# Optimization experiments

Hardware: AMD Instinct MI355X
Metric: run time of the kernel (lower is better)

Reference implementation:

```python
import jax, jax.numpy as jnp
import numpy as np

N, D, K = 10240, 256, 30  # nodes, feature dim, top-k
EPS = 1e-12  # F.normalize eps


def setup_inputs() -> dict:
    key = jax.random.key(0)
    k1, _ = jax.random.split(key)
    features = jax.random.normal(k1, (N, D), dtype=jnp.float32)
    # Attentive layers: elementwise feature weights, initialized to ones (as in the repo)
    w1 = jnp.ones((D,), dtype=jnp.float32)
    w2 = jnp.ones((D,), dtype=jnp.float32)
    return {"features": features, "w1": w1, "w2": w2, "k": K}


def reference(features, w1, w2, k):
    # internal_forward: Attentive = x * w (x @ diag(w)); relu between layers (mlp_act='relu')
    h = jax.nn.relu(features * w1) * w2              # [N, D]
    # F.normalize(dim=1, p=2) with eps clamp
    norm = jnp.maximum(jnp.linalg.norm(h, axis=1, keepdims=True), EPS)
    emb = h / norm                                   # [N, D]
    # cal_similarity_graph: dense cosine similarity
    sim = emb @ emb.T                                # [N, N]
    # top_k(sim, k+1): keep top (k+1) entries per row, zero the rest
    _, idx = jax.lax.top_k(sim, k + 1)               # [N, k+1]
    rows = jnp.arange(sim.shape[0])[:, None]
    mask = jnp.zeros_like(sim).at[rows, idx].set(1.0)
    # apply_non_linearity with 'relu'
    return jax.nn.relu(sim * mask)
```

## Files before the change

### kernel.cpp

```cpp
#include <hip/hip_runtime.h>
#include <math.h>

#define N_NODES 10240
#define DIM 256
#define TPB 256
#define CAP 1536

typedef _Float16 half8 __attribute__((ext_vector_type(8)));
typedef float f32x4 __attribute__((ext_vector_type(4)));

__device__ __forceinline__ void async_load16(const void* g, void* l) {
  __builtin_amdgcn_global_load_lds(
      (const __attribute__((address_space(1))) unsigned int*)g,
      (__attribute__((address_space(3))) unsigned int*)l, 16, 0, 0);
}

__device__ __forceinline__ unsigned int fmap(float f) {
  unsigned int s = __float_as_uint(f);
  return (s & 0x80000000u) ? ~s : (s | 0x80000000u);
}
__device__ __forceinline__ float funmap(unsigned int m) {
  return __uint_as_float((m & 0x80000000u) ? (m ^ 0x80000000u) : ~m);
}

__global__ __launch_bounds__(256) void norm_split_kernel(
    const float* __restrict__ F, const float* __restrict__ w1,
    const float* __restrict__ w2, _Float16* __restrict__ P0,
    _Float16* __restrict__ P1) {
  int row = blockIdx.x, tid = threadIdx.x;
  __shared__ float red[TPB];
  size_t base = (size_t)row * DIM + tid;
  float h = fmaxf(F[base] * w1[tid], 0.0f) * w2[tid];
  red[tid] = h * h;
  __syncthreads();
  for (int o = TPB / 2; o > 0; o >>= 1) {
    if (tid < o) red[tid] += red[tid + o];
    __syncthreads();
  }
  float e = h / fmaxf(sqrtf(red[0]), 1e-12f);
  _Float16 p0 = (_Float16)e;
  _Float16 p1 = (_Float16)((e - (float)p0) * 2048.0f);
  P0[base] = p0;
  P1[base] = p1;
}

__global__ __launch_bounds__(256) void gemm_mfma_kernel(
    const _Float16* __restrict__ P0, const _Float16* __restrict__ P1,
    float* __restrict__ C) {
  __shared__ char smem[32768];
  char* AsB = smem;
  char* BsB = smem + 16384;

  int tid = threadIdx.x;
  int lane = tid & 63;
  int w = tid >> 6;
  int wr = (w >> 1) * 64;
  int wc = (w & 1) * 64;
  int quad = lane >> 4;
  int mr = lane & 15;
  int rowBase = blockIdx.y * 128;
  int colBase = blockIdx.x * 128;

  size_t rowOffA[4], rowOffB[4];
  int ldsOff[4];
#pragma unroll
  for (int i = 0; i < 4; ++i) {
    int u = tid + i * 256;
    int m = u >> 3;
    int g = (u & 7) ^ (m & 7);
    ldsOff[i] = u * 16;
    rowOffA[i] = (size_t)(rowBase + m) * DIM + g * 8;
    rowOffB[i] = (size_t)(colBase + m) * DIM + g * 8;
  }

  int fOffA[2][4], fOffB[2][4];
#pragma unroll
  for (int s = 0; s < 2; ++s)
#pragma unroll
    for (int t = 0; t < 4; ++t) {
      int g = s * 4 + quad;
      int mA = wr + t * 16 + mr;
      fOffA[s][t] = (mA * 8 + (g ^ (mA & 7))) * 16;
      int mB = wc + t * 16 + mr;
      fOffB[s][t] = (mB * 8 + (g ^ (mB & 7))) * 16;
    }

  f32x4 acc[4][4];
#pragma unroll
  for (int t = 0; t < 4; ++t)
#pragma unroll
    for (int u2 = 0; u2 < 4; ++u2) acc[t][u2] = (f32x4)0.0f;

  const _Float16* Aseg[3] = {P0, P1, P0};
  const _Float16* Bseg[3] = {P1, P0, P0};

  for (int pass = 0; pass < 3; ++pass) {
    if (pass == 2) {
      const float sc = 1.0f / 2048.0f;
#pragma unroll
      for (int t = 0; t < 4; ++t)
#pragma unroll
        for (int u2 = 0; u2 < 4; ++u2)
#pragma unroll
          for (int r = 0; r < 4; ++r) acc[t][u2][r] *= sc;
    }
    const _Float16* Ap = Aseg[pass];
    const _Float16* Bp = Bseg[pass];
    for (int c = 0; c < 4; ++c) {
      int kb = c * 64;
#pragma unroll
      for (int i = 0; i < 4; ++i)
        async_load16(Ap + rowOffA[i] + kb, AsB + ldsOff[i]);
#pragma unroll
      for (int i = 0; i < 4; ++i)
        async_load16(Bp + rowOffB[i] + kb, BsB + ldsOff[i]);
      __syncthreads();
#pragma unroll
      for (int s = 0; s < 2; ++s) {
        half8 af[4], bf[4];
#pragma unroll
        for (int t = 0; t < 4; ++t) {
          af[t] = *(const half8*)(AsB + fOffA[s][t]);
          bf[t] = *(const half8*)(BsB + fOffB[s][t]);
        }
#pragma unroll
        for (int t = 0; t < 4; ++t)
#pragma unroll
          for (int u2 = 0; u2 < 4; ++u2)
            acc[t][u2] = __builtin_amdgcn_mfma_f32_16x16x32_f16(
                af[t], bf[u2], acc[t][u2], 0, 0, 0);
      }
      __syncthreads();
    }
  }

#pragma unroll
  for (int t = 0; t < 4; ++t) {
    int gr = rowBase + wr + t * 16 + quad * 4;
#pragma unroll
    for (int u2 = 0; u2 < 4; ++u2) {
      int gc = colBase + wc + u2 * 16 + mr;
      float* cp = C + (size_t)gr * N_NODES + gc;
      cp[0] = acc[t][u2][0];
      cp[(size_t)N_NODES] = acc[t][u2][1];
      cp[(size_t)2 * N_NODES] = acc[t][u2][2];
      cp[(size_t)3 * N_NODES] = acc[t][u2][3];
    }
  }
}

__global__ __launch_bounds__(256) void topk_sparse_kernel(
    const float* __restrict__ SIM, float* __restrict__ OUT,
    const int* __restrict__ kptr) {
  constexpr int EPT = N_NODES / TPB;
  constexpr int NV4 = EPT / 4;
  __shared__ unsigned int lm[TPB];
  __shared__ unsigned int cu[CAP];
  __shared__ int ci[CAP];
  __shared__ unsigned int s_cnt, s_L31, s_Tu;
  __shared__ int s_Jcut;

  int tid = threadIdx.x;
  const float* Srow = SIM + (size_t)blockIdx.x * N_NODES;
  float* Orow = OUT + (size_t)blockIdx.x * N_NODES;
  unsigned int want = (unsigned int)(kptr[0] + 1);

  unsigned int u[EPT];
  unsigned int lmax = 0u;
#pragma unroll
  for (int i = 0; i < NV4; ++i) {
    float4 v = *(const float4*)&Srow[(i * TPB + tid) * 4];
    float fv[4] = {v.x, v.y, v.z, v.w};
#pragma unroll
    for (int c = 0; c < 4; ++c) {
      unsigned int m = fmap(fv[c]);
      u[i * 4 + c] = m;
      lmax = (m > lmax) ? m : lmax;
    }
  }
  lm[tid] = lmax;
  if (tid == 0) s_cnt = 0u;
  __syncthreads();

  {
    unsigned int r = 0;
    for (int j = 0; j < TPB; ++j) {
      unsigned int vj = lm[j];
      r += (vj > lmax) || (vj == lmax && j < tid);
    }
    if (r == want - 1) s_L31 = lmax;
  }
  __syncthreads();
  unsigned int L31 = s_L31;

#pragma unroll
  for (int i = 0; i < EPT; ++i) {
    if (u[i] >= L31) {
      unsigned int pos = atomicAdd(&s_cnt, 1u);
      if (pos < CAP) {
        cu[pos] = u[i];
        ci[pos] = ((i / 4) * TPB + tid) * 4 + (i % 4);
      }
    }
  }
  __syncthreads();
  unsigned int c_total = s_cnt;

  if (c_total <= CAP) {
    for (unsigned int i = tid; i < c_total; i += TPB) {
      unsigned int ui = cu[i];
      int ii = ci[i];
      unsigned int r = 0;
      for (unsigned int j = 0; j < c_total; ++j) {
        unsigned int uj = cu[j];
        r += (uj > ui) || (uj == ui && ci[j] < ii);
      }
      if (r == want - 1) { s_Tu = ui; s_Jcut = ii; }
    }
    __syncthreads();
  } else {
    unsigned int lo = 0u, hi = 0xFFFFFFFFu;
    while (lo < hi) {
      unsigned int mid = lo + ((hi - lo) >> 1);
      unsigned int cnt = 0;
#pragma unroll
      for (int i = 0; i < EPT; ++i) cnt += (u[i] > mid) ? 1u : 0u;
      lm[tid] = cnt;
      __syncthreads();
      for (int o = TPB / 2; o > 0; o >>= 1) {
        if (tid < o) lm[tid] += lm[tid + o];
        __syncthreads();
      }
      unsigned int gcnt = lm[0];
      __syncthreads();
      if (gcnt < want) hi = mid; else lo = mid + 1u;
    }
    unsigned int Tu = lo;
    unsigned int cnt = 0;
#pragma unroll
    for (int i = 0; i < EPT; ++i) cnt += (u[i] > Tu) ? 1u : 0u;
    lm[tid] = cnt;
    __syncthreads();
    for (int o = TPB / 2; o > 0; o >>= 1) {
      if (tid < o) lm[tid] += lm[tid + o];
      __syncthreads();
    }
    unsigned int need = want - lm[0];
    __syncthreads();
    int jlo = 0, jhi = N_NODES - 1;
    while (jlo < jhi) {
      int jmid = (jlo + jhi) >> 1;
      unsigned int cc = 0;
#pragma unroll
      for (int i = 0; i < EPT; ++i) {
        int jj = ((i / 4) * TPB + tid) * 4 + (i % 4);
        cc += (u[i] == Tu && jj <= jmid) ? 1u : 0u;
      }
      lm[tid] = cc;
      __syncthreads();
      for (int o = TPB / 2; o > 0; o >>= 1) {
        if (tid < o) lm[tid] += lm[tid + o];
        __syncthreads();
      }
      unsigned int tot = lm[0];
      __syncthreads();
      if (tot >= need) jhi = jmid; else jlo = jmid + 1;
    }
    if (tid == 0) { s_Tu = Tu; s_Jcut = jlo; }
    __syncthreads();
  }

  unsigned int Tu = s_Tu;
  int Jcut = s_Jcut;

#pragma unroll
  for (int i = 0; i < EPT; ++i) {
    unsigned int m = u[i];
    int j = ((i / 4) * TPB + tid) * 4 + (i % 4);
    bool keep = (m > Tu) || (m == Tu && j <= Jcut);
    if (keep) {
      float v = funmap(m);
      if (v > 0.0f) Orow[j] = v;
    }
  }
}

__global__ __launch_bounds__(256) void topk_kernel(
    float* __restrict__ C, const int* __restrict__ kptr) {
  constexpr int EPT = N_NODES / TPB;
  constexpr int NV4 = EPT / 4;
  __shared__ unsigned int lm[TPB];
  __shared__ unsigned int cu[CAP];
  __shared__ int ci[CAP];
  __shared__ unsigned int s_cnt, s_L31, s_Tu;
  __shared__ int s_Jcut;

  int tid = threadIdx.x;
  float* Crow = C + (size_t)blockIdx.x * N_NODES;
  unsigned int want = (unsigned int)(kptr[0] + 1);

  unsigned int u[EPT];
  unsigned int lmax = 0u;
#pragma unroll
  for (int i = 0; i < NV4; ++i) {
    float4 v = *(const float4*)&Crow[(i * TPB + tid) * 4];
    float fv[4] = {v.x, v.y, v.z, v.w};
#pragma unroll
    for (int c = 0; c < 4; ++c) {
      unsigned int m = fmap(fv[c]);
      u[i * 4 + c] = m;
      lmax = (m > lmax) ? m : lmax;
    }
  }
  lm[tid] = lmax;
  if (tid == 0) s_cnt = 0u;
  __syncthreads();

  {
    unsigned int r = 0;
    for (int j = 0; j < TPB; ++j) {
      unsigned int vj = lm[j];
      r += (vj > lmax) || (vj == lmax && j < tid);
    }
    if (r == want - 1) s_L31 = lmax;
  }
  __syncthreads();
  unsigned int L31 = s_L31;

#pragma unroll
  for (int i = 0; i < EPT; ++i) {
    if (u[i] >= L31) {
      unsigned int pos = atomicAdd(&s_cnt, 1u);
      if (pos < CAP) {
        cu[pos] = u[i];
        ci[pos] = ((i / 4) * TPB + tid) * 4 + (i % 4);
      }
    }
  }
  __syncthreads();
  unsigned int c_total = s_cnt;

  if (c_total <= CAP) {
    for (unsigned int i = tid; i < c_total; i += TPB) {
      unsigned int ui = cu[i];
      int ii = ci[i];
      unsigned int r = 0;
      for (unsigned int j = 0; j < c_total; ++j) {
        unsigned int uj = cu[j];
        r += (uj > ui) || (uj == ui && ci[j] < ii);
      }
      if (r == want - 1) { s_Tu = ui; s_Jcut = ii; }
    }
    __syncthreads();
  } else {
    unsigned int lo = 0u, hi = 0xFFFFFFFFu;
    while (lo < hi) {
      unsigned int mid = lo + ((hi - lo) >> 1);
      unsigned int cnt = 0;
#pragma unroll
      for (int i = 0; i < EPT; ++i) cnt += (u[i] > mid) ? 1u : 0u;
      lm[tid] = cnt;
      __syncthreads();
      for (int o = TPB / 2; o > 0; o >>= 1) {
        if (tid < o) lm[tid] += lm[tid + o];
        __syncthreads();
      }
      unsigned int gcnt = lm[0];
      __syncthreads();
      if (gcnt < want) hi = mid; else lo = mid + 1u;
    }
    unsigned int Tu = lo;
    unsigned int cnt = 0;
#pragma unroll
    for (int i = 0; i < EPT; ++i) cnt += (u[i] > Tu) ? 1u : 0u;
    lm[tid] = cnt;
    __syncthreads();
    for (int o = TPB / 2; o > 0; o >>= 1) {
      if (tid < o) lm[tid] += lm[tid + o];
      __syncthreads();
    }
    unsigned int need = want - lm[0];
    __syncthreads();
    int jlo = 0, jhi = N_NODES - 1;
    while (jlo < jhi) {
      int jmid = (jlo + jhi) >> 1;
      unsigned int cc = 0;
#pragma unroll
      for (int i = 0; i < EPT; ++i) {
        int jj = ((i / 4) * TPB + tid) * 4 + (i % 4);
        cc += (u[i] == Tu && jj <= jmid) ? 1u : 0u;
      }
      lm[tid] = cc;
      __syncthreads();
      for (int o = TPB / 2; o > 0; o >>= 1) {
        if (tid < o) lm[tid] += lm[tid + o];
        __syncthreads();
      }
      unsigned int tot = lm[0];
      __syncthreads();
      if (tot >= need) jhi = jmid; else jlo = jmid + 1;
    }
    if (tid == 0) { s_Tu = Tu; s_Jcut = jlo; }
    __syncthreads();
  }

  unsigned int Tu = s_Tu;
  int Jcut = s_Jcut;

#pragma unroll
  for (int i = 0; i < NV4; ++i) {
    float out[4];
#pragma unroll
    for (int c = 0; c < 4; ++c) {
      unsigned int m = u[i * 4 + c];
      int j = (i * TPB + tid) * 4 + c;
      bool keep = (m > Tu) || (m == Tu && j <= Jcut);
      float v = funmap(m);
      out[c] = (keep && v > 0.0f) ? v : 0.0f;
    }
    *(float4*)&Crow[(i * TPB + tid) * 4] =
        make_float4(out[0], out[1], out[2], out[3]);
  }
}

extern "C" void kernel_launch(void* const* d_in, const int* in_sizes, int n_in,
                              void* d_out, int out_size, void* d_ws, size_t ws_size,
                              hipStream_t stream) {
  const float* F  = (const float*)d_in[0];
  const float* w1 = (const float*)d_in[1];
  const float* w2 = (const float*)d_in[2];
  const int*   kp = (const int*)d_in[3];
  float* C = (float*)d_out;
  _Float16* P0 = (_Float16*)d_ws;
  _Float16* P1 = P0 + (size_t)N_NODES * DIM;

  size_t pbytes = (size_t)N_NODES * DIM * sizeof(_Float16);
  size_t simoff = 2 * pbytes;
  size_t need = simoff + (size_t)N_NODES * N_NODES * sizeof(float);

  dim3 grid(N_NODES / 128, N_NODES / 128);

  norm_split_kernel<<<N_NODES, DIM, 0, stream>>>(F, w1, w2, P0, P1);

  if (ws_size >= need) {
    float* SIM = (float*)((char*)d_ws + simoff);
    gemm_mfma_kernel<<<grid, 256, 0, stream>>>(P0, P1, SIM);
    topk_sparse_kernel<<<N_NODES, TPB, 0, stream>>>(SIM, C, kp);
  } else {
    gemm_mfma_kernel<<<grid, 256, 0, stream>>>(P0, P1, C);
    topk_kernel<<<N_NODES, TPB, 0, stream>>>(C, kp);
  }
}
```

Measured before the change: 655.2 us.

## Emit per-tile row maxima from GEMM and prune top-k to candidate tiles

The GEMM epilogue now reduces each 128x128 tile's accumulators to a per-row maximum and writes these into an extra workspace array of 80 tile maxima per row. The top-k kernel ranks those 80 maxima to find a threshold and only reads the column tiles whose maximum reaches it, rather than streaming the full 10240-wide similarity row. Candidates are then ranked exactly and scattered from shared memory. It adds a shared-memory reduction and sync to the GEMM tail and needs more workspace, and it falls back to a full-row bisection when the candidate count overflows.

```diff
diff --git a/kernel.cpp b/kernel.cpp
--- a/kernel.cpp
+++ b/kernel.cpp
@@ -5,6 +5,8 @@
 #define DIM 256
 #define TPB 256
 #define CAP 1536
+#define CAP2 2048
+#define NTILE 80
 
 typedef _Float16 half8 __attribute__((ext_vector_type(8)));
 typedef float f32x4 __attribute__((ext_vector_type(4)));
@@ -46,8 +48,8 @@
 
 __global__ __launch_bounds__(256) void gemm_mfma_kernel(
     const _Float16* __restrict__ P0, const _Float16* __restrict__ P1,
-    float* __restrict__ C) {
-  __shared__ char smem[32768];
+    float* __restrict__ C, float* __restrict__ TM) {
+  __shared__ __align__(16) char smem[32768];
   char* AsB = smem;
   char* BsB = smem + 16384;
 
@@ -147,78 +149,116 @@
       cp[(size_t)3 * N_NODES] = acc[t][u2][3];
     }
   }
-}
-
-__global__ __launch_bounds__(256) void topk_sparse_kernel(
-    const float* __restrict__ SIM, float* __restrict__ OUT,
-    const int* __restrict__ kptr) {
+
+  if (TM != nullptr) {
+    float* red = (float*)smem;
+    int half = w & 1;
+#pragma unroll
+    for (int t = 0; t < 4; ++t)
+#pragma unroll
+      for (int r = 0; r < 4; ++r) {
+        float m = fmaxf(fmaxf(acc[t][0][r], acc[t][1][r]),
+                        fmaxf(acc[t][2][r], acc[t][3][r]));
+        m = fmaxf(m, __shfl_xor(m, 1, 64));
+        m = fmaxf(m, __shfl_xor(m, 2, 64));
+        m = fmaxf(m, __shfl_xor(m, 4, 64));
+        m = fmaxf(m, __shfl_xor(m, 8, 64));
+        if (mr == 0) red[half * 128 + wr + t * 16 + quad * 4 + r] = m;
+      }
+    __syncthreads();
+    if (tid < 64) {
+      float a0 = fmaxf(red[2 * tid], red[128 + 2 * tid]);
+      float a1 = fmaxf(red[2 * tid + 1], red[128 + 2 * tid + 1]);
+      *(float2*)(TM + (size_t)blockIdx.x * N_NODES + rowBase + 2 * tid) =
+          make_float2(a0, a1);
+    }
+  }
+}
+
+__global__ __launch_bounds__(256) void topk_tile_kernel(
+    const float* __restrict__ SIM, const float* __restrict__ TM,
+    float* __restrict__ OUT, const int* __restrict__ kptr) {
   constexpr int EPT = N_NODES / TPB;
   constexpr int NV4 = EPT / 4;
+  __shared__ unsigned int sm[NTILE];
+  __shared__ unsigned char qlist[NTILE];
+  __shared__ unsigned int cu[CAP2];
+  __shared__ int ci[CAP2];
   __shared__ unsigned int lm[TPB];
-  __shared__ unsigned int cu[CAP];
-  __shared__ int ci[CAP];
-  __shared__ unsigned int s_cnt, s_L31, s_Tu;
+  __shared__ unsigned int s_cnt, s_q, s_Tp, s_Tu;
   __shared__ int s_Jcut;
 
   int tid = threadIdx.x;
-  const float* Srow = SIM + (size_t)blockIdx.x * N_NODES;
-  float* Orow = OUT + (size_t)blockIdx.x * N_NODES;
+  int row = blockIdx.x;
+  const float* Srow = SIM + (size_t)row * N_NODES;
+  float* Orow = OUT + (size_t)row * N_NODES;
   unsigned int want = (unsigned int)(kptr[0] + 1);
 
-  unsigned int u[EPT];
-  unsigned int lmax = 0u;
-#pragma unroll
-  for (int i = 0; i < NV4; ++i) {
-    float4 v = *(const float4*)&Srow[(i * TPB + tid) * 4];
-    float fv[4] = {v.x, v.y, v.z, v.w};
-#pragma unroll
-    for (int c = 0; c < 4; ++c) {
-      unsigned int m = fmap(fv[c]);
-      u[i * 4 + c] = m;
-      lmax = (m > lmax) ? m : lmax;
-    }
-  }
-  lm[tid] = lmax;
-  if (tid == 0) s_cnt = 0u;
-  __syncthreads();
-
-  {
+  if (tid == 0) { s_cnt = 0u; s_q = 0u; s_Tp = 0u; }
+  if (tid < NTILE) sm[tid] = fmap(TM[(size_t)tid * N_NODES + row]);
+  __syncthreads();
+
+  if (want <= NTILE && tid < NTILE) {
+    unsigned int mv = sm[tid];
     unsigned int r = 0;
-    for (int j = 0; j < TPB; ++j) {
-      unsigned int vj = lm[j];
-      r += (vj > lmax) || (vj == lmax && j < tid);
-    }
-    if (r == want - 1) s_L31 = lmax;
-  }
-  __syncthreads();
-  unsigned int L31 = s_L31;
-
-#pragma unroll
-  for (int i = 0; i < EPT; ++i) {
-    if (u[i] >= L31) {
-      unsigned int pos = atomicAdd(&s_cnt, 1u);
-      if (pos < CAP) {
-        cu[pos] = u[i];
-        ci[pos] = ((i / 4) * TPB + tid) * 4 + (i % 4);
-      }
-    }
-  }
-  __syncthreads();
-  unsigned int c_total = s_cnt;
-
-  if (c_total <= CAP) {
-    for (unsigned int i = tid; i < c_total; i += TPB) {
+    for (int j = 0; j < NTILE; ++j) {
+      unsigned int vj = sm[j];
+      r += (vj > mv) || (vj == mv && j < tid);
+    }
+    if (r == want - 1) s_Tp = mv;
+  }
+  __syncthreads();
+  unsigned int Tp = s_Tp;
+
+  if (tid < NTILE && sm[tid] >= Tp)
+    qlist[atomicAdd(&s_q, 1u)] = (unsigned char)tid;
+  __syncthreads();
+  unsigned int nq = s_q;
+
+  for (unsigned int idx = tid; idx < nq * 128u; idx += TPB) {
+    int tile = qlist[idx >> 7];
+    int col = tile * 128 + (int)(idx & 127u);
+    unsigned int m = fmap(Srow[col]);
+    if (m >= Tp) {
+      unsigned int p = atomicAdd(&s_cnt, 1u);
+      if (p < CAP2) { cu[p] = m; ci[p] = col; }
+    }
+  }
+  __syncthreads();
+  unsigned int ct = s_cnt;
+
+  if (ct <= CAP2) {
+    for (unsigned int i = tid; i < ct; i += TPB) {
       unsigned int ui = cu[i];
       int ii = ci[i];
       unsigned int r = 0;
-      for (unsigned int j = 0; j < c_total; ++j) {
+      for (unsigned int j = 0; j < ct; ++j) {
         unsigned int uj = cu[j];
         r += (uj > ui) || (uj == ui && ci[j] < ii);
       }
       if (r == want - 1) { s_Tu = ui; s_Jcut = ii; }
     }
     __syncthreads();
+    unsigned int Tu = s_Tu;
+    int Jcut = s_Jcut;
+    for (unsigned int i = tid; i < ct; i += TPB) {
+      unsigned int m = cu[i];
+      int col = ci[i];
+      bool keep = (m > Tu) || (m == Tu && col <= Jcut);
+      if (keep) {
+        float v = funmap(m);
+        if (v > 0.0f) Orow[col] = v;
+      }
+    }
   } else {
+    unsigned int u[EPT];
+#pragma unroll
+    for (int i = 0; i < NV4; ++i) {
+      float4 v = *(const float4*)&Srow[(i * TPB + tid) * 4];
+      float fv[4] = {v.x, v.y, v.z, v.w};
+#pragma unroll
+      for (int c = 0; c < 4; ++c) u[i * 4 + c] = fmap(fv[c]);
+    }
     unsigned int lo = 0u, hi = 0xFFFFFFFFu;
     while (lo < hi) {
       unsigned int mid = lo + ((hi - lo) >> 1);
@@ -266,21 +306,15 @@
       __syncthreads();
       if (tot >= need) jhi = jmid; else jlo = jmid + 1;
     }
-    if (tid == 0) { s_Tu = Tu; s_Jcut = jlo; }
-    __syncthreads();
-  }
-
-  unsigned int Tu = s_Tu;
-  int Jcut = s_Jcut;
-
-#pragma unroll
-  for (int i = 0; i < EPT; ++i) {
-    unsigned int m = u[i];
-    int j = ((i / 4) * TPB + tid) * 4 + (i % 4);
-    bool keep = (m > Tu) || (m == Tu && j <= Jcut);
-    if (keep) {
-      float v = funmap(m);
-      if (v > 0.0f) Orow[j] = v;
+#pragma unroll
+    for (int i = 0; i < EPT; ++i) {
+      unsigned int m = u[i];
+      int j = ((i / 4) * TPB + tid) * 4 + (i % 4);
+      bool keep = (m > Tu) || (m == Tu && j <= jlo);
+      if (keep) {
+        float v = funmap(m);
+        if (v > 0.0f) Orow[j] = v;
+      }
     }
   }
 }
@@ -436,7 +470,9 @@
 
   size_t pbytes = (size_t)N_NODES * DIM * sizeof(_Float16);
   size_t simoff = 2 * pbytes;
-  size_t need = simoff + (size_t)N_NODES * N_NODES * sizeof(float);
+  size_t simbytes = (size_t)N_NODES * N_NODES * sizeof(float);
+  size_t tmoff = simoff + simbytes;
+  size_t need = tmoff + (size_t)NTILE * N_NODES * sizeof(float);
 
   dim3 grid(N_NODES / 128, N_NODES / 128);
 
@@ -444,10 +480,11 @@
 
   if (ws_size >= need) {
     float* SIM = (float*)((char*)d_ws + simoff);
-    gemm_mfma_kernel<<<grid, 256, 0, stream>>>(P0, P1, SIM);
-    topk_sparse_kernel<<<N_NODES, TPB, 0, stream>>>(SIM, C, kp);
+    float* TM  = (float*)((char*)d_ws + tmoff);
+    gemm_mfma_kernel<<<grid, 256, 0, stream>>>(P0, P1, SIM, TM);
+    topk_tile_kernel<<<N_NODES, TPB, 0, stream>>>(SIM, TM, C, kp);
   } else {
-    gemm_mfma_kernel<<<grid, 256, 0, stream>>>(P0, P1, C);
+    gemm_mfma_kernel<<<grid, 256, 0, stream>>>(P0, P1, C, nullptr);
     topk_kernel<<<N_NODES, TPB, 0, stream>>>(C, kp);
   }
 }
```

Measured after the change: 694.9 us. 6.0% more time.

## Double-buffer LDS tiles in MFMA GEMM to overlap loads with compute

Applied to the files above, without the earlier changes.

Replaces the three-pass, four-chunk load-sync-compute loop with a flattened twelve-stage loop. It uses two 32KB LDS buffers, prefetching the next stage's A/B tiles via async global-to-LDS loads while computing on the current one. This aims to hide global load latency behind MFMA work and drops one barrier per stage. LDS use doubles to 64KB per block, which may reduce occupancy. Correctness depends on the async loads completing before the single barrier at the end of each stage.

```diff
diff --git a/kernel.cpp b/kernel.cpp
--- a/kernel.cpp
+++ b/kernel.cpp
@@ -47,9 +47,7 @@
 __global__ __launch_bounds__(256) void gemm_mfma_kernel(
     const _Float16* __restrict__ P0, const _Float16* __restrict__ P1,
     float* __restrict__ C) {
-  __shared__ char smem[32768];
-  char* AsB = smem;
-  char* BsB = smem + 16384;
+  __shared__ __align__(16) char smem[65536];
 
   int tid = threadIdx.x;
   int lane = tid & 63;
@@ -91,11 +89,27 @@
 #pragma unroll
     for (int u2 = 0; u2 < 4; ++u2) acc[t][u2] = (f32x4)0.0f;
 
-  const _Float16* Aseg[3] = {P0, P1, P0};
-  const _Float16* Bseg[3] = {P1, P0, P0};
-
-  for (int pass = 0; pass < 3; ++pass) {
-    if (pass == 2) {
+#define ISSUE_STAGE(sidx, buf)                                            \
+  do {                                                                    \
+    const _Float16* Ap_ = ((sidx) >> 2 == 1) ? P1 : P0;                   \
+    const _Float16* Bp_ = ((sidx) >> 2 == 0) ? P1 : P0;                   \
+    int kb_ = ((sidx) & 3) * 64;                                          \
+    char* base_ = smem + (buf) * 32768;                                   \
+    _Pragma("unroll")                                                     \
+    for (int i_ = 0; i_ < 4; ++i_)                                        \
+      async_load16(Ap_ + rowOffA[i_] + kb_, base_ + ldsOff[i_]);          \
+    _Pragma("unroll")                                                     \
+    for (int i_ = 0; i_ < 4; ++i_)                                        \
+      async_load16(Bp_ + rowOffB[i_] + kb_, base_ + 16384 + ldsOff[i_]);  \
+  } while (0)
+
+  ISSUE_STAGE(0, 0);
+  __syncthreads();
+
+  int cur = 0;
+  for (int sidx = 0; sidx < 12; ++sidx) {
+    if (sidx < 11) ISSUE_STAGE(sidx + 1, cur ^ 1);
+    if (sidx == 8) {
       const float sc = 1.0f / 2048.0f;
 #pragma unroll
       for (int t = 0; t < 4; ++t)
@@ -104,35 +118,27 @@
 #pragma unroll
           for (int r = 0; r < 4; ++r) acc[t][u2][r] *= sc;
     }
-    const _Float16* Ap = Aseg[pass];
-    const _Float16* Bp = Bseg[pass];
-    for (int c = 0; c < 4; ++c) {
-      int kb = c * 64;
-#pragma unroll
-      for (int i = 0; i < 4; ++i)
-        async_load16(Ap + rowOffA[i] + kb, AsB + ldsOff[i]);
-#pragma unroll
-      for (int i = 0; i < 4; ++i)
-        async_load16(Bp + rowOffB[i] + kb, BsB + ldsOff[i]);
-      __syncthreads();
-#pragma unroll
-      for (int s = 0; s < 2; ++s) {
-        half8 af[4], bf[4];
-#pragma unroll
-        for (int t = 0; t < 4; ++t) {
-          af[t] = *(const half8*)(AsB + fOffA[s][t]);
-          bf[t] = *(const half8*)(BsB + fOffB[s][t]);
-        }
-#pragma unroll
-        for (int t = 0; t < 4; ++t)
-#pragma unroll
-          for (int u2 = 0; u2 < 4; ++u2)
-            acc[t][u2] = __builtin_amdgcn_mfma_f32_16x16x32_f16(
-                af[t], bf[u2], acc[t][u2], 0, 0, 0);
-      }
-      __syncthreads();
-    }
-  }
+    char* Ab = smem + cur * 32768;
+    char* Bb = Ab + 16384;
+#pragma unroll
+    for (int s = 0; s < 2; ++s) {
+      half8 af[4], bf[4];
+#pragma unroll
+      for (int t = 0; t < 4; ++t) {
+        af[t] = *(const half8*)(Ab + fOffA[s][t]);
+        bf[t] = *(const half8*)(Bb + fOffB[s][t]);
+      }
+#pragma unroll
+      for (int t = 0; t < 4; ++t)
+#pragma unroll
+        for (int u2 = 0; u2 < 4; ++u2)
+          acc[t][u2] = __builtin_amdgcn_mfma_f32_16x16x32_f16(
+              af[t], bf[u2], acc[t][u2], 0, 0, 0);
+    }
+    __syncthreads();
+    cur ^= 1;
+  }
+#undef ISSUE_STAGE
 
 #pragma unroll
   for (int t = 0; t < 4; ++t) {
```

Result: slower. 689.1 us (+5.2%).
